# Optimization experiments

Hardware: AMD Instinct MI355X
Metric: run time of the kernel (lower is better)

Reference implementation:

```python
import jax, jax.numpy as jnp
import numpy as np

N_NODES = 100000
N_HYPEREDGES = 50000
N_CAND = 200000
SET_SIZE = 8
EMB_DIM = 64


def setup_inputs() -> dict:
    key = jax.random.key(0)
    k1, k2, k3, k4 = jax.random.split(key, 4)
    node_emb = jax.random.normal(k1, (N_NODES, EMB_DIM), dtype=jnp.float32)
    hyperedge_emb = jax.random.normal(k2, (N_HYPEREDGES, EMB_DIM), dtype=jnp.float32)
    h = jax.random.randint(k3, (N_CAND,), 0, N_HYPEREDGES, dtype=jnp.int64)
    X = jax.random.randint(k4, (N_CAND, SET_SIZE), 0, N_NODES, dtype=jnp.int64)
    return {"node_emb": node_emb, "hyperedge_emb": hyperedge_emb, "h": h, "X": X}


def reference(node_emb, hyperedge_emb, h, X):
    # Gather per-candidate embeddings
    src = hyperedge_emb[h]          # [E, d]
    embs = node_emb[X]              # [E, S, d]

    # star_: min over nodes of sigmoid(<hyperedge, node>)
    star_scores = jax.nn.sigmoid(jnp.einsum('ed,esd->es', src, embs))  # [E, S]
    star = jnp.min(star_scores, axis=1, keepdims=True)                 # [E, 1]

    # clique_: min over all pairs of sigmoid(<node_i, node_j>)
    pair_scores = jax.nn.sigmoid(jnp.einsum('esd,etd->est', embs, embs))  # [E, S, S]
    clique = jnp.min(pair_scores, axis=(1, 2), keepdims=False)[:, None]   # [E, 1]

    return jnp.concatenate([star, clique], axis=-1)  # [E, 2]
```

## Files before the change

kernel.cpp:

```cpp
#include <hip/hip_runtime.h>
#include <hip/hip_fp16.h>
#include <math.h>

#define SET_SIZE 8
#define EMB_DIM 64
#define NPAIR 36
#define NDOT (SET_SIZE + NPAIR)

typedef _Float16 f16x2 __attribute__((ext_vector_type(2)));

union Frag16 {
    float4 f4;
    f16x2  h2[4];
};

__device__ __forceinline__ float dot8_f16(const Frag16& a, const Frag16& b, float c) {
#if __has_builtin(__builtin_amdgcn_fdot2)
    c = __builtin_amdgcn_fdot2(a.h2[0], b.h2[0], c, false);
    c = __builtin_amdgcn_fdot2(a.h2[1], b.h2[1], c, false);
    c = __builtin_amdgcn_fdot2(a.h2[2], b.h2[2], c, false);
    c = __builtin_amdgcn_fdot2(a.h2[3], b.h2[3], c, false);
#else
#pragma unroll
    for (int j = 0; j < 4; ++j) {
        c = fmaf((float)a.h2[j].x, (float)b.h2[j].x, c);
        c = fmaf((float)a.h2[j].y, (float)b.h2[j].y, c);
    }
#endif
    return c;
}

__global__ __launch_bounds__(256) void cvt_f32_f16_kernel(
    const float* __restrict__ in, __half* __restrict__ out, int n8)
{
    int i = blockIdx.x * blockDim.x + threadIdx.x;
    if (i >= n8) return;
    const float4* p = (const float4*)in + 2 * (size_t)i;
    float4 a = p[0], b = p[1];
    union { __half2 h2[4]; float4 f4; } u;
    u.h2[0] = __floats2half2_rn(a.x, a.y);
    u.h2[1] = __floats2half2_rn(a.z, a.w);
    u.h2[2] = __floats2half2_rn(b.x, b.y);
    u.h2[3] = __floats2half2_rn(b.z, b.w);
    ((float4*)out)[i] = u.f4;
}

__global__ __launch_bounds__(256) void hyperedge_score_f16(
    const __half* __restrict__ node_f16,
    const __half* __restrict__ he_f16,
    const int*    __restrict__ h,
    const int*    __restrict__ X,
    float*        __restrict__ out,
    int n_cand)
{
    int tid = blockIdx.x * blockDim.x + threadIdx.x;
    int grp = tid >> 3;
    int q   = tid & 7;
    if (grp >= n_cand) return;

    const int4* Xv = (const int4*)(X + (size_t)grp * SET_SIZE);
    int4 x0 = Xv[0];
    int4 x1 = Xv[1];
    int he = h[grp];
    int idx[SET_SIZE] = {x0.x, x0.y, x0.z, x0.w, x1.x, x1.y, x1.z, x1.w};

    Frag16 v[9];
#pragma unroll
    for (int r = 0; r < SET_SIZE; ++r)
        v[r].f4 = *((const float4*)(node_f16 + (size_t)idx[r] * EMB_DIM) + q);
    v[8].f4 = *((const float4*)(he_f16 + (size_t)he * EMB_DIM) + q);

    float acc[NDOT];
#pragma unroll
    for (int s = 0; s < SET_SIZE; ++s)
        acc[s] = dot8_f16(v[8], v[s], 0.0f);
    {
        int k = SET_SIZE;
#pragma unroll
        for (int s = 0; s < SET_SIZE; ++s) {
#pragma unroll
            for (int t = s; t < SET_SIZE; ++t, ++k)
                acc[k] = dot8_f16(v[s], v[t], 0.0f);
        }
    }

#pragma unroll
    for (int i = 0; i < NDOT; ++i) {
        float x = acc[i];
        x += __shfl_xor(x, 1);
        x += __shfl_xor(x, 2);
        x += __shfl_xor(x, 4);
        acc[i] = x;
    }

    float smin = acc[0];
#pragma unroll
    for (int s = 1; s < SET_SIZE; ++s) smin = fminf(smin, acc[s]);
    float pmin = acc[SET_SIZE];
#pragma unroll
    for (int i = 1; i < NPAIR; ++i) pmin = fminf(pmin, acc[SET_SIZE + i]);

    float res = (q == 0) ? 1.0f / (1.0f + __expf(-smin))
                         : 1.0f / (1.0f + __expf(-pmin));
    if (q < 2) out[(size_t)grp * 2 + q] = res;
}

__device__ __forceinline__ float dot4f(float4 a, float4 b) {
    return fmaf(a.x, b.x, fmaf(a.y, b.y, fmaf(a.z, b.z, a.w * b.w)));
}

__global__ __launch_bounds__(256) void hyperedge_score_f32(
    const float* __restrict__ node_emb, const float* __restrict__ hyperedge_emb,
    const int* __restrict__ h, const int* __restrict__ X,
    float* __restrict__ out, int n_cand)
{
    int tid = blockIdx.x * blockDim.x + threadIdx.x;
    int grp = tid >> 3;
    int q   = tid & 7;
    if (grp >= n_cand) return;
    const int4* Xv = (const int4*)(X + (size_t)grp * SET_SIZE);
    int4 x0 = Xv[0]; int4 x1 = Xv[1];
    int he = h[grp];
    int idx[SET_SIZE] = {x0.x, x0.y, x0.z, x0.w, x1.x, x1.y, x1.z, x1.w};
    float4 va[9], vb[9];
#pragma unroll
    for (int r = 0; r < SET_SIZE; ++r) {
        const float4* p = (const float4*)(node_emb + (size_t)idx[r] * EMB_DIM) + 2 * q;
        va[r] = p[0]; vb[r] = p[1];
    }
    {
        const float4* p = (const float4*)(hyperedge_emb + (size_t)he * EMB_DIM) + 2 * q;
        va[8] = p[0]; vb[8] = p[1];
    }
    float acc[NDOT];
#pragma unroll
    for (int s = 0; s < SET_SIZE; ++s)
        acc[s] = dot4f(va[8], va[s]) + dot4f(vb[8], vb[s]);
    {
        int k = SET_SIZE;
#pragma unroll
        for (int s = 0; s < SET_SIZE; ++s)
#pragma unroll
            for (int t = s; t < SET_SIZE; ++t, ++k)
                acc[k] = dot4f(va[s], va[t]) + dot4f(vb[s], vb[t]);
    }
#pragma unroll
    for (int i = 0; i < NDOT; ++i) {
        float x = acc[i];
        x += __shfl_xor(x, 1);
        x += __shfl_xor(x, 2);
        x += __shfl_xor(x, 4);
        acc[i] = x;
    }
    float smin = acc[0];
#pragma unroll
    for (int s = 1; s < SET_SIZE; ++s) smin = fminf(smin, acc[s]);
    float pmin = acc[SET_SIZE];
#pragma unroll
    for (int i = 1; i < NPAIR; ++i) pmin = fminf(pmin, acc[SET_SIZE + i]);
    float res = (q == 0) ? 1.0f / (1.0f + __expf(-smin))
                         : 1.0f / (1.0f + __expf(-pmin));
    if (q < 2) out[(size_t)grp * 2 + q] = res;
}

extern "C" void kernel_launch(void* const* d_in, const int* in_sizes, int n_in,
                              void* d_out, int out_size, void* d_ws, size_t ws_size,
                              hipStream_t stream) {
    const float* node_emb      = (const float*)d_in[0];
    const float* hyperedge_emb = (const float*)d_in[1];
    const int*   h             = (const int*)d_in[2];
    const int*   X             = (const int*)d_in[3];
    float*       out           = (float*)d_out;

    int n_node_elems = in_sizes[0];
    int n_he_elems   = in_sizes[1];
    int n_cand       = in_sizes[2];

    size_t need = ((size_t)n_node_elems + (size_t)n_he_elems) * sizeof(__half);
    int block = 256;
    long long total_threads = (long long)n_cand * 8;
    int grid_main = (int)((total_threads + block - 1) / block);

    if (ws_size >= need) {
        __half* node_f16 = (__half*)d_ws;
        __half* he_f16   = node_f16 + n_node_elems;

        int n8_node = n_node_elems / 8;
        int n8_he   = n_he_elems / 8;
        cvt_f32_f16_kernel<<<(n8_node + block - 1) / block, block, 0, stream>>>(
            node_emb, node_f16, n8_node);
        cvt_f32_f16_kernel<<<(n8_he + block - 1) / block, block, 0, stream>>>(
            hyperedge_emb, he_f16, n8_he);

        hyperedge_score_f16<<<grid_main, block, 0, stream>>>(
            node_f16, he_f16, h, X, out, n_cand);
    } else {
        hyperedge_score_f32<<<grid_main, block, 0, stream>>>(
            node_emb, hyperedge_emb, h, X, out, n_cand);
    }
}
```

Measured before the change: 125.6 us.

## Use 4 lanes per candidate with DPP quad reduction and fused conversion kernel

Each candidate is now handled by 4 lanes instead of 8. Every lane loads two 16-byte fp16 chunks per row and runs 8 fdot2 steps per dot product. The cross-lane sum uses DPP quad permutes instead of three shfl_xor rounds, and the two f32-to-f16 conversion launches are merged into one. This halves the reduction work and the lane count per candidate and removes a launch, at the cost of more registers per lane (launch_bounds 256,3).

After: 114.7 us. 8.6% less time.

```diff
diff --git a/kernel.cpp b/kernel.cpp
--- a/kernel.cpp
+++ b/kernel.cpp
@@ -9,43 +9,48 @@
 
 typedef _Float16 f16x2 __attribute__((ext_vector_type(2)));
 
-union Frag16 {
-    float4 f4;
-    f16x2  h2[4];
+union Frag32 {
+    float4 f4[2];
+    f16x2  h2[8];
 };
 
-__device__ __forceinline__ float dot8_f16(const Frag16& a, const Frag16& b, float c) {
-#if __has_builtin(__builtin_amdgcn_fdot2)
-    c = __builtin_amdgcn_fdot2(a.h2[0], b.h2[0], c, false);
-    c = __builtin_amdgcn_fdot2(a.h2[1], b.h2[1], c, false);
-    c = __builtin_amdgcn_fdot2(a.h2[2], b.h2[2], c, false);
-    c = __builtin_amdgcn_fdot2(a.h2[3], b.h2[3], c, false);
-#else
-#pragma unroll
-    for (int j = 0; j < 4; ++j) {
-        c = fmaf((float)a.h2[j].x, (float)b.h2[j].x, c);
-        c = fmaf((float)a.h2[j].y, (float)b.h2[j].y, c);
-    }
-#endif
+__device__ __forceinline__ float dot16_f16(const Frag32& a, const Frag32& b, float c) {
+#pragma unroll
+    for (int j = 0; j < 8; ++j)
+        c = __builtin_amdgcn_fdot2(a.h2[j], b.h2[j], c, false);
     return c;
 }
 
-__global__ __launch_bounds__(256) void cvt_f32_f16_kernel(
-    const float* __restrict__ in, __half* __restrict__ out, int n8)
+__device__ __forceinline__ float quad_reduce_add(float x) {
+    int t = __builtin_amdgcn_update_dpp(0, __float_as_int(x), 0xB1, 0xF, 0xF, true);
+    x += __int_as_float(t);
+    t = __builtin_amdgcn_update_dpp(0, __float_as_int(x), 0x4E, 0xF, 0xF, true);
+    x += __int_as_float(t);
+    return x;
+}
+
+__global__ __launch_bounds__(256) void cvt_both_kernel(
+    const float* __restrict__ a, const float* __restrict__ b,
+    __half* __restrict__ oa, __half* __restrict__ ob, int n8a, int n8b)
 {
     int i = blockIdx.x * blockDim.x + threadIdx.x;
-    if (i >= n8) return;
-    const float4* p = (const float4*)in + 2 * (size_t)i;
-    float4 a = p[0], b = p[1];
+    const float* in;
+    __half* out;
+    int j;
+    if (i < n8a) { in = a; out = oa; j = i; }
+    else if (i < n8a + n8b) { in = b; out = ob; j = i - n8a; }
+    else return;
+    const float4* p = (const float4*)in + 2 * (size_t)j;
+    float4 x = p[0], y = p[1];
     union { __half2 h2[4]; float4 f4; } u;
-    u.h2[0] = __floats2half2_rn(a.x, a.y);
-    u.h2[1] = __floats2half2_rn(a.z, a.w);
-    u.h2[2] = __floats2half2_rn(b.x, b.y);
-    u.h2[3] = __floats2half2_rn(b.z, b.w);
-    ((float4*)out)[i] = u.f4;
-}
-
-__global__ __launch_bounds__(256) void hyperedge_score_f16(
+    u.h2[0] = __floats2half2_rn(x.x, x.y);
+    u.h2[1] = __floats2half2_rn(x.z, x.w);
+    u.h2[2] = __floats2half2_rn(y.x, y.y);
+    u.h2[3] = __floats2half2_rn(y.z, y.w);
+    ((float4*)out)[j] = u.f4;
+}
+
+__global__ __launch_bounds__(256, 3) void hyperedge_score_q4(
     const __half* __restrict__ node_f16,
     const __half* __restrict__ he_f16,
     const int*    __restrict__ h,
@@ -54,8 +59,8 @@
     int n_cand)
 {
     int tid = blockIdx.x * blockDim.x + threadIdx.x;
-    int grp = tid >> 3;
-    int q   = tid & 7;
+    int grp = tid >> 2;
+    int q   = tid & 3;
     if (grp >= n_cand) return;
 
     const int4* Xv = (const int4*)(X + (size_t)grp * SET_SIZE);
@@ -64,34 +69,36 @@
     int he = h[grp];
     int idx[SET_SIZE] = {x0.x, x0.y, x0.z, x0.w, x1.x, x1.y, x1.z, x1.w};
 
-    Frag16 v[9];
-#pragma unroll
-    for (int r = 0; r < SET_SIZE; ++r)
-        v[r].f4 = *((const float4*)(node_f16 + (size_t)idx[r] * EMB_DIM) + q);
-    v[8].f4 = *((const float4*)(he_f16 + (size_t)he * EMB_DIM) + q);
+    Frag32 v[9];
+#pragma unroll
+    for (int r = 0; r < SET_SIZE; ++r) {
+        const float4* p = (const float4*)(node_f16 + (size_t)idx[r] * EMB_DIM);
+        v[r].f4[0] = p[q];
+        v[r].f4[1] = p[q + 4];
+    }
+    {
+        const float4* p = (const float4*)(he_f16 + (size_t)he * EMB_DIM);
+        v[8].f4[0] = p[q];
+        v[8].f4[1] = p[q + 4];
+    }
 
     float acc[NDOT];
 #pragma unroll
     for (int s = 0; s < SET_SIZE; ++s)
-        acc[s] = dot8_f16(v[8], v[s], 0.0f);
+        acc[s] = dot16_f16(v[8], v[s], 0.0f);
     {
         int k = SET_SIZE;
 #pragma unroll
         for (int s = 0; s < SET_SIZE; ++s) {
 #pragma unroll
             for (int t = s; t < SET_SIZE; ++t, ++k)
-                acc[k] = dot8_f16(v[s], v[t], 0.0f);
+                acc[k] = dot16_f16(v[s], v[t], 0.0f);
         }
     }
 
 #pragma unroll
-    for (int i = 0; i < NDOT; ++i) {
-        float x = acc[i];
-        x += __shfl_xor(x, 1);
-        x += __shfl_xor(x, 2);
-        x += __shfl_xor(x, 4);
-        acc[i] = x;
-    }
+    for (int i = 0; i < NDOT; ++i)
+        acc[i] = quad_reduce_add(acc[i]);
 
     float smin = acc[0];
 #pragma unroll
@@ -178,8 +185,6 @@
 
     size_t need = ((size_t)n_node_elems + (size_t)n_he_elems) * sizeof(__half);
     int block = 256;
-    long long total_threads = (long long)n_cand * 8;
-    int grid_main = (int)((total_threads + block - 1) / block);
 
     if (ws_size >= need) {
         __half* node_f16 = (__half*)d_ws;
@@ -187,14 +192,17 @@
 
         int n8_node = n_node_elems / 8;
         int n8_he   = n_he_elems / 8;
-        cvt_f32_f16_kernel<<<(n8_node + block - 1) / block, block, 0, stream>>>(
-            node_emb, node_f16, n8_node);
-        cvt_f32_f16_kernel<<<(n8_he + block - 1) / block, block, 0, stream>>>(
-            hyperedge_emb, he_f16, n8_he);
-
-        hyperedge_score_f16<<<grid_main, block, 0, stream>>>(
+        int n8_tot  = n8_node + n8_he;
+        cvt_both_kernel<<<(n8_tot + block - 1) / block, block, 0, stream>>>(
+            node_emb, hyperedge_emb, node_f16, he_f16, n8_node, n8_he);
+
+        long long total_threads = (long long)n_cand * 4;
+        int grid_main = (int)((total_threads + block - 1) / block);
+        hyperedge_score_q4<<<grid_main, block, 0, stream>>>(
             node_f16, he_f16, h, X, out, n_cand);
     } else {
+        long long total_threads = (long long)n_cand * 8;
+        int grid_main = (int)((total_threads + block - 1) / block);
         hyperedge_score_f32<<<grid_main, block, 0, stream>>>(
             node_emb, hyperedge_emb, h, X, out, n_cand);
     }
```
